# Optimization experiments

Hardware: AMD Instinct MI355X
Metric: run time of the kernel (lower is better)

The kernel has to match this reference:

```python
import jax, jax.numpy as jnp
import numpy as np

B, N, D_IN, D_MEM, LAYERS = 8, 2048, 128, 128, 3


def setup_inputs() -> dict:
    key = jax.random.key(0)
    k1, k2, k3, k4 = jax.random.split(key, 4)
    inputs = jax.random.normal(k1, (B, N, D_IN), dtype=jnp.float32)
    # attention-derived adjacency: nonnegative weights
    out_adj = jax.random.uniform(k2, (B, N, N), dtype=jnp.float32)
    # per-layer Linear weights (all layers 128->128 here, stacked) with
    # torch nn.Linear-style init scale 1/sqrt(fan_in)
    scale = 1.0 / np.sqrt(D_IN)
    W = jax.random.uniform(k3, (LAYERS, D_IN, D_MEM), minval=-scale, maxval=scale, dtype=jnp.float32)
    b = jax.random.uniform(k4, (LAYERS, D_MEM), minval=-scale, maxval=scale, dtype=jnp.float32)
    return {"inputs": inputs, "out_adj": out_adj, "W": W, "b": b}


def reference(inputs, out_adj, W, b):
    # GCN.forward (eval mode; dropout = identity)
    adj = out_adj  # [B, N, N]
    denom = jnp.sum(adj, axis=2, keepdims=True) + 1.0  # [B, N, 1]
    outputs = inputs  # [B, N, D]
    for l in range(W.shape[0]):
        Ax = jnp.einsum('bij,bjd->bid', adj, outputs)      # aggregate
        AxW = Ax @ W[l] + b[l]                             # per-layer linear
        outputs = jax.nn.relu(AxW / denom)                 # normalize + activate
    return outputs
```

## Files before the change

kernel.cpp:

```cpp
#include <hip/hip_runtime.h>

#define NN 2048
#define DD 128
#define BK 128
#define NT (NN / BK)

typedef _Float16 f16x8 __attribute__((ext_vector_type(8)));
typedef float f32x4 __attribute__((ext_vector_type(4)));

__global__ __launch_bounds__(256) void prep_kernel(
    const float* __restrict__ W, _Float16* __restrict__ Wt) {
  int idx = blockIdx.x * 256 + threadIdx.x;
  int l = idx >> 14, r = idx & 16383, d = r >> 7, k = r & 127;
  Wt[idx] = (_Float16)W[l * 16384 + k * 128 + d];
}

__global__ __launch_bounds__(256) void gemmY_kernel(
    const float* __restrict__ X, const _Float16* __restrict__ Wt,
    _Float16* __restrict__ Yt) {
  const int bx = blockIdx.x;
  const int batch = bx & 7, n0 = (bx >> 3) * 32;
  const int tid = threadIdx.x, lane = tid & 63, wave = tid >> 6;
  const int quad = lane >> 4, l15 = lane & 15, d0 = wave * 32;
  f32x4 acc[2][2] = {};
#pragma unroll
  for (int kk = 0; kk < 128; kk += 32) {
    f16x8 a0 = *(const f16x8*)(Wt + (d0 + l15) * DD + kk + quad * 8);
    f16x8 a1 = *(const f16x8*)(Wt + (d0 + 16 + l15) * DD + kk + quad * 8);
#pragma unroll
    for (int fi = 0; fi < 2; ++fi) {
      const float* xp = X + (size_t)(batch * NN + n0 + fi * 16 + l15) * DD + kk + quad * 8;
      float4 x0 = *(const float4*)xp;
      float4 x1 = *(const float4*)(xp + 4);
      f16x8 b = {(_Float16)x0.x, (_Float16)x0.y, (_Float16)x0.z, (_Float16)x0.w,
                 (_Float16)x1.x, (_Float16)x1.y, (_Float16)x1.z, (_Float16)x1.w};
      acc[0][fi] = __builtin_amdgcn_mfma_f32_16x16x32_f16(a0, b, acc[0][fi], 0, 0, 0);
      acc[1][fi] = __builtin_amdgcn_mfma_f32_16x16x32_f16(a1, b, acc[1][fi], 0, 0, 0);
    }
  }
  _Float16* YtB = Yt + (size_t)batch * DD * NN;
#pragma unroll
  for (int df = 0; df < 2; ++df)
#pragma unroll
    for (int fi = 0; fi < 2; ++fi)
#pragma unroll
      for (int r = 0; r < 4; ++r)
        YtB[(size_t)(d0 + df * 16 + quad * 4 + r) * NN + n0 + fi * 16 + l15] =
            (_Float16)acc[df][fi][r];
}

template<bool LAST>
__global__ __launch_bounds__(256, 2) void agg_kernel(
    const float* __restrict__ adj, const _Float16* __restrict__ Yt,
    const float* __restrict__ bias, const _Float16* __restrict__ Wn,
    _Float16* __restrict__ Ytn, float* __restrict__ out) {
  __shared__ __align__(16) float Bsm[2][32 * BK];
  float* acts = &Bsm[0][0];
  __shared__ float bsh[128];

  const int tid = threadIdx.x, bx = blockIdx.x;
  const int batch = bx & 7, i0 = (bx >> 3) * 32;
  const int wave = tid >> 6, lane = tid & 63;
  const int quad = lane >> 4, l15 = lane & 15;
  const int d0 = wave * 32;
  const int l31 = lane & 31, lh = lane >> 5;

  const float* adjB = adj + (size_t)(batch * NN + i0) * NN;
  const _Float16* YA0 = Yt + (size_t)batch * DD * NN + (size_t)(d0 + l15) * NN + quad * 8;
  const _Float16* YA1 = YA0 + (size_t)16 * NN;

  if (tid < 128) bsh[tid] = bias[tid];

  f32x4 acc[2][2] = {};
  float rs0 = 0.f, rs1 = 0.f;

  auto STAGE = [&](int ko, int buf) {
#pragma unroll
    for (int u = 0; u < 4; ++u) {
      const int rt = wave * 8 + u * 2 + lh;
      const float* g = adjB + (size_t)rt * NN + ko * BK + ((l31 ^ (rt & 7)) << 2);
      __builtin_amdgcn_global_load_lds(
          (const __attribute__((address_space(1))) unsigned int*)g,
          (__attribute__((address_space(3))) unsigned int*)
              &Bsm[buf][(wave * 8 + u * 2) * BK],
          16, 0, 0);
    }
  };

  STAGE(0, 0);
  __syncthreads();

  for (int ko = 0; ko < NT; ++ko) {
    const int buf = ko & 1;
    if (ko + 1 < NT) STAGE(ko + 1, buf ^ 1);
    f16x8 a[4][2];
#pragma unroll
    for (int kk = 0; kk < 4; ++kk) {
      a[kk][0] = *(const f16x8*)(YA0 + ko * BK + kk * 32);
      a[kk][1] = *(const f16x8*)(YA1 + ko * BK + kk * 32);
    }
    const float* Bt = Bsm[buf];
#pragma unroll
    for (int kk = 0; kk < 4; ++kk) {
#pragma unroll
      for (int fi = 0; fi < 2; ++fi) {
        const int row = fi * 16 + l15;
        const int c0 = kk * 8 + quad * 2;
        const float* rp = Bt + row * BK;
        float4 w0 = *(const float4*)(rp + ((c0 ^ (row & 7)) << 2));
        float4 w1 = *(const float4*)(rp + (((c0 + 1) ^ (row & 7)) << 2));
        float s = ((w0.x + w0.y) + (w0.z + w0.w)) + ((w1.x + w1.y) + (w1.z + w1.w));
        if (fi == 0) rs0 += s; else rs1 += s;
        f16x8 b = {(_Float16)w0.x, (_Float16)w0.y, (_Float16)w0.z, (_Float16)w0.w,
                   (_Float16)w1.x, (_Float16)w1.y, (_Float16)w1.z, (_Float16)w1.w};
        acc[0][fi] = __builtin_amdgcn_mfma_f32_16x16x32_f16(a[kk][0], b, acc[0][fi], 0, 0, 0);
        acc[1][fi] = __builtin_amdgcn_mfma_f32_16x16x32_f16(a[kk][1], b, acc[1][fi], 0, 0, 0);
      }
    }
    __syncthreads();
  }

  rs0 += __shfl_xor(rs0, 16); rs0 += __shfl_xor(rs0, 32);
  rs1 += __shfl_xor(rs1, 16); rs1 += __shfl_xor(rs1, 32);
  const float rdv0 = 1.0f / (rs0 + 1.0f);
  const float rdv1 = 1.0f / (rs1 + 1.0f);

#pragma unroll
  for (int af = 0; af < 2; ++af)
#pragma unroll
    for (int r = 0; r < 4; ++r) {
      const int d = d0 + af * 16 + quad * 4 + r;
      const float bv = bsh[d];
      acts[l15 * 132 + d]        = fmaxf((acc[af][0][r] + bv) * rdv0, 0.f);
      acts[(16 + l15) * 132 + d] = fmaxf((acc[af][1][r] + bv) * rdv1, 0.f);
    }
  __syncthreads();

  if (LAST) {
    float* ob = out + (size_t)(batch * NN + i0) * DD;
#pragma unroll
    for (int u = 0; u < 4; ++u) {
      int c = tid + 256 * u;
      int i = c >> 5, f4 = (c & 31) * 4;
      *(float4*)(ob + (size_t)i * DD + f4) = *(const float4*)&acts[i * 132 + f4];
    }
  } else {
    f32x4 acc2[2][2] = {};
#pragma unroll
    for (int kk = 0; kk < 128; kk += 32) {
      f16x8 a0 = *(const f16x8*)(Wn + (d0 + l15) * DD + kk + quad * 8);
      f16x8 a1 = *(const f16x8*)(Wn + (d0 + 16 + l15) * DD + kk + quad * 8);
#pragma unroll
      for (int fi = 0; fi < 2; ++fi) {
        const float* xp = &acts[(fi * 16 + l15) * 132 + kk + quad * 8];
        float4 x0 = *(const float4*)xp;
        float4 x1 = *(const float4*)(xp + 4);
        f16x8 b = {(_Float16)x0.x, (_Float16)x0.y, (_Float16)x0.z, (_Float16)x0.w,
                   (_Float16)x1.x, (_Float16)x1.y, (_Float16)x1.z, (_Float16)x1.w};
        acc2[0][fi] = __builtin_amdgcn_mfma_f32_16x16x32_f16(a0, b, acc2[0][fi], 0, 0, 0);
        acc2[1][fi] = __builtin_amdgcn_mfma_f32_16x16x32_f16(a1, b, acc2[1][fi], 0, 0, 0);
      }
    }
    _Float16* YnB = Ytn + (size_t)batch * DD * NN;
#pragma unroll
    for (int af = 0; af < 2; ++af)
#pragma unroll
      for (int fi = 0; fi < 2; ++fi)
#pragma unroll
        for (int r = 0; r < 4; ++r)
          YnB[(size_t)(d0 + af * 16 + quad * 4 + r) * NN + i0 + fi * 16 + l15] =
              (_Float16)acc2[af][fi][r];
  }
}

extern "C" void kernel_launch(void* const* d_in, const int* in_sizes, int n_in,
                              void* d_out, int out_size, void* d_ws, size_t ws_size,
                              hipStream_t stream) {
  const float* x0   = (const float*)d_in[0];
  const float* adj  = (const float*)d_in[1];
  const float* W    = (const float*)d_in[2];
  const float* bias = (const float*)d_in[3];
  float* out = (float*)d_out;

  char* ws = (char*)d_ws;
  _Float16* Wt  = (_Float16*)ws;
  _Float16* Yt0 = (_Float16*)(ws + (1u << 20));
  _Float16* Yt1 = (_Float16*)(ws + 6u * (1u << 20));

  prep_kernel <<<192, 256, 0, stream>>>(W, Wt);
  gemmY_kernel<<<512, 256, 0, stream>>>(x0, Wt, Yt0);
  agg_kernel<false><<<512, 256, 0, stream>>>(adj, Yt0, bias,       Wt + 16384, Yt1, nullptr);
  agg_kernel<false><<<512, 256, 0, stream>>>(adj, Yt1, bias + 128, Wt + 32768, Yt0, nullptr);
  agg_kernel<true ><<<512, 256, 0, stream>>>(adj, Yt0, bias + 256, nullptr,    nullptr, out);
}
```

Before: 303.4 us.

## Use single-wave agg blocks with register-prefetched global loads instead of LDS staging

```diff
diff --git a/kernel.cpp b/kernel.cpp
--- a/kernel.cpp
+++ b/kernel.cpp
@@ -2,8 +2,6 @@
 
 #define NN 2048
 #define DD 128
-#define BK 128
-#define NT (NN / BK)
 
 typedef _Float16 f16x8 __attribute__((ext_vector_type(8)));
 typedef float f32x4 __attribute__((ext_vector_type(4)));
@@ -50,126 +48,139 @@
 }
 
 template<bool LAST>
-__global__ __launch_bounds__(256, 2) void agg_kernel(
+__global__ __launch_bounds__(64, 1) void agg_kernel(
     const float* __restrict__ adj, const _Float16* __restrict__ Yt,
     const float* __restrict__ bias, const _Float16* __restrict__ Wn,
     _Float16* __restrict__ Ytn, float* __restrict__ out) {
-  __shared__ __align__(16) float Bsm[2][32 * BK];
-  float* acts = &Bsm[0][0];
-  __shared__ float bsh[128];
-
-  const int tid = threadIdx.x, bx = blockIdx.x;
+  __shared__ _Float16 acts[32][136];
+  __shared__ float rd[32];
+
+  const int bx = blockIdx.x;
   const int batch = bx & 7, i0 = (bx >> 3) * 32;
-  const int wave = tid >> 6, lane = tid & 63;
+  const int lane = threadIdx.x & 63;
   const int quad = lane >> 4, l15 = lane & 15;
-  const int d0 = wave * 32;
-  const int l31 = lane & 31, lh = lane >> 5;
-
-  const float* adjB = adj + (size_t)(batch * NN + i0) * NN;
-  const _Float16* YA0 = Yt + (size_t)batch * DD * NN + (size_t)(d0 + l15) * NN + quad * 8;
-  const _Float16* YA1 = YA0 + (size_t)16 * NN;
-
-  if (tid < 128) bsh[tid] = bias[tid];
-
-  f32x4 acc[2][2] = {};
+
+  const float* A0p = adj + (size_t)(batch * NN + i0 + l15) * NN + quad * 8;
+  const float* A1p = A0p + (size_t)16 * NN;
+  const _Float16* Yb = Yt + (size_t)batch * DD * NN + (size_t)l15 * NN + quad * 8;
+
+  f32x4 acc[2][8] = {};
   float rs0 = 0.f, rs1 = 0.f;
 
-  auto STAGE = [&](int ko, int buf) {
+  float4 pa[4][4];
+  f16x8 py[4][8];
+
+#define LOADS(jj, st)                                                   \
+  do {                                                                  \
+    pa[st][0] = *(const float4*)(A0p + (jj));                           \
+    pa[st][1] = *(const float4*)(A0p + (jj) + 4);                       \
+    pa[st][2] = *(const float4*)(A1p + (jj));                           \
+    pa[st][3] = *(const float4*)(A1p + (jj) + 4);                       \
+    _Pragma("unroll")                                                   \
+    for (int f = 0; f < 8; ++f)                                         \
+      py[st][f] = *(const f16x8*)(Yb + (size_t)(f * 16) * NN + (jj));   \
+  } while (0)
+
+#define COMPUTE(st)                                                     \
+  do {                                                                  \
+    float4 a00 = pa[st][0], a01 = pa[st][1];                            \
+    float4 a10 = pa[st][2], a11 = pa[st][3];                            \
+    f16x8 y[8];                                                         \
+    _Pragma("unroll")                                                   \
+    for (int f = 0; f < 8; ++f) y[f] = py[st][f];                       \
+    rs0 += ((a00.x + a00.y) + (a00.z + a00.w)) +                        \
+           ((a01.x + a01.y) + (a01.z + a01.w));                         \
+    rs1 += ((a10.x + a10.y) + (a10.z + a10.w)) +                        \
+           ((a11.x + a11.y) + (a11.z + a11.w));                         \
+    f16x8 af0 = {(_Float16)a00.x, (_Float16)a00.y, (_Float16)a00.z,     \
+                 (_Float16)a00.w, (_Float16)a01.x, (_Float16)a01.y,     \
+                 (_Float16)a01.z, (_Float16)a01.w};                     \
+    f16x8 af1 = {(_Float16)a10.x, (_Float16)a10.y, (_Float16)a10.z,     \
+                 (_Float16)a10.w, (_Float16)a11.x, (_Float16)a11.y,     \
+                 (_Float16)a11.z, (_Float16)a11.w};                     \
+    _Pragma("unroll")                                                   \
+    for (int f = 0; f < 8; ++f) {                                       \
+      acc[0][f] = __builtin_amdgcn_mfma_f32_16x16x32_f16(af0, y[f], acc[0][f], 0, 0, 0); \
+      acc[1][f] = __builtin_amdgcn_mfma_f32_16x16x32_f16(af1, y[f], acc[1][f], 0, 0, 0); \
+    }                                                                   \
+  } while (0)
+
+  LOADS(0, 0); LOADS(32, 1); LOADS(64, 2); LOADS(96, 3);
+
+  for (int j = 0; j < NN - 128; j += 128) {
 #pragma unroll
     for (int u = 0; u < 4; ++u) {
-      const int rt = wave * 8 + u * 2 + lh;
-      const float* g = adjB + (size_t)rt * NN + ko * BK + ((l31 ^ (rt & 7)) << 2);
-      __builtin_amdgcn_global_load_lds(
-          (const __attribute__((address_space(1))) unsigned int*)g,
-          (__attribute__((address_space(3))) unsigned int*)
-              &Bsm[buf][(wave * 8 + u * 2) * BK],
-          16, 0, 0);
+      COMPUTE(u);
+      LOADS(j + u * 32 + 128, u);
     }
-  };
-
-  STAGE(0, 0);
+  }
+#pragma unroll
+  for (int u = 0; u < 4; ++u) COMPUTE(u);
+#undef LOADS
+#undef COMPUTE
+
+  rs0 += __shfl_xor(rs0, 16); rs0 += __shfl_xor(rs0, 32);
+  rs1 += __shfl_xor(rs1, 16); rs1 += __shfl_xor(rs1, 32);
+  if (lane < 16) {
+    rd[l15] = 1.0f / (rs0 + 1.0f);
+    rd[16 + l15] = 1.0f / (rs1 + 1.0f);
+  }
   __syncthreads();
 
-  for (int ko = 0; ko < NT; ++ko) {
-    const int buf = ko & 1;
-    if (ko + 1 < NT) STAGE(ko + 1, buf ^ 1);
-    f16x8 a[4][2];
-#pragma unroll
-    for (int kk = 0; kk < 4; ++kk) {
-      a[kk][0] = *(const f16x8*)(YA0 + ko * BK + kk * 32);
-      a[kk][1] = *(const f16x8*)(YA1 + ko * BK + kk * 32);
-    }
-    const float* Bt = Bsm[buf];
-#pragma unroll
-    for (int kk = 0; kk < 4; ++kk) {
-#pragma unroll
-      for (int fi = 0; fi < 2; ++fi) {
-        const int row = fi * 16 + l15;
-        const int c0 = kk * 8 + quad * 2;
-        const float* rp = Bt + row * BK;
-        float4 w0 = *(const float4*)(rp + ((c0 ^ (row & 7)) << 2));
-        float4 w1 = *(const float4*)(rp + (((c0 + 1) ^ (row & 7)) << 2));
-        float s = ((w0.x + w0.y) + (w0.z + w0.w)) + ((w1.x + w1.y) + (w1.z + w1.w));
-        if (fi == 0) rs0 += s; else rs1 += s;
-        f16x8 b = {(_Float16)w0.x, (_Float16)w0.y, (_Float16)w0.z, (_Float16)w0.w,
-                   (_Float16)w1.x, (_Float16)w1.y, (_Float16)w1.z, (_Float16)w1.w};
-        acc[0][fi] = __builtin_amdgcn_mfma_f32_16x16x32_f16(a[kk][0], b, acc[0][fi], 0, 0, 0);
-        acc[1][fi] = __builtin_amdgcn_mfma_f32_16x16x32_f16(a[kk][1], b, acc[1][fi], 0, 0, 0);
+  float bv[8];
+#pragma unroll
+  for (int f = 0; f < 8; ++f) bv[f] = bias[f * 16 + l15];
+  float rdv[2][4];
+#pragma unroll
+  for (int fi = 0; fi < 2; ++fi)
+#pragma unroll
+    for (int r = 0; r < 4; ++r) rdv[fi][r] = rd[fi * 16 + quad * 4 + r];
+
+  if (LAST) {
+    float* ob = out + (size_t)(batch * NN + i0) * DD;
+#pragma unroll
+    for (int fi = 0; fi < 2; ++fi)
+#pragma unroll
+      for (int f = 0; f < 8; ++f)
+#pragma unroll
+        for (int r = 0; r < 4; ++r) {
+          int i = fi * 16 + quad * 4 + r;
+          ob[(size_t)i * DD + f * 16 + l15] =
+              fmaxf((acc[fi][f][r] + bv[f]) * rdv[fi][r], 0.f);
+        }
+  } else {
+#pragma unroll
+    for (int fi = 0; fi < 2; ++fi)
+#pragma unroll
+      for (int f = 0; f < 8; ++f)
+#pragma unroll
+        for (int r = 0; r < 4; ++r) {
+          int i = fi * 16 + quad * 4 + r;
+          acts[i][f * 16 + l15] =
+              (_Float16)fmaxf((acc[fi][f][r] + bv[f]) * rdv[fi][r], 0.f);
+        }
+    __syncthreads();
+    f32x4 acc2[8][2] = {};
+#pragma unroll
+    for (int kk = 0; kk < 128; kk += 32) {
+      f16x8 b0 = *(const f16x8*)&acts[l15][kk + quad * 8];
+      f16x8 b1 = *(const f16x8*)&acts[16 + l15][kk + quad * 8];
+#pragma unroll
+      for (int m = 0; m < 8; ++m) {
+        f16x8 aw = *(const f16x8*)(Wn + (m * 16 + l15) * DD + kk + quad * 8);
+        acc2[m][0] = __builtin_amdgcn_mfma_f32_16x16x32_f16(aw, b0, acc2[m][0], 0, 0, 0);
+        acc2[m][1] = __builtin_amdgcn_mfma_f32_16x16x32_f16(aw, b1, acc2[m][1], 0, 0, 0);
       }
     }
-    __syncthreads();
-  }
-
-  rs0 += __shfl_xor(rs0, 16); rs0 += __shfl_xor(rs0, 32);
-  rs1 += __shfl_xor(rs1, 16); rs1 += __shfl_xor(rs1, 32);
-  const float rdv0 = 1.0f / (rs0 + 1.0f);
-  const float rdv1 = 1.0f / (rs1 + 1.0f);
-
-#pragma unroll
-  for (int af = 0; af < 2; ++af)
-#pragma unroll
-    for (int r = 0; r < 4; ++r) {
-      const int d = d0 + af * 16 + quad * 4 + r;
-      const float bv = bsh[d];
-      acts[l15 * 132 + d]        = fmaxf((acc[af][0][r] + bv) * rdv0, 0.f);
-      acts[(16 + l15) * 132 + d] = fmaxf((acc[af][1][r] + bv) * rdv1, 0.f);
-    }
-  __syncthreads();
-
-  if (LAST) {
-    float* ob = out + (size_t)(batch * NN + i0) * DD;
-#pragma unroll
-    for (int u = 0; u < 4; ++u) {
-      int c = tid + 256 * u;
-      int i = c >> 5, f4 = (c & 31) * 4;
-      *(float4*)(ob + (size_t)i * DD + f4) = *(const float4*)&acts[i * 132 + f4];
-    }
-  } else {
-    f32x4 acc2[2][2] = {};
-#pragma unroll
-    for (int kk = 0; kk < 128; kk += 32) {
-      f16x8 a0 = *(const f16x8*)(Wn + (d0 + l15) * DD + kk + quad * 8);
-      f16x8 a1 = *(const f16x8*)(Wn + (d0 + 16 + l15) * DD + kk + quad * 8);
-#pragma unroll
-      for (int fi = 0; fi < 2; ++fi) {
-        const float* xp = &acts[(fi * 16 + l15) * 132 + kk + quad * 8];
-        float4 x0 = *(const float4*)xp;
-        float4 x1 = *(const float4*)(xp + 4);
-        f16x8 b = {(_Float16)x0.x, (_Float16)x0.y, (_Float16)x0.z, (_Float16)x0.w,
-                   (_Float16)x1.x, (_Float16)x1.y, (_Float16)x1.z, (_Float16)x1.w};
-        acc2[0][fi] = __builtin_amdgcn_mfma_f32_16x16x32_f16(a0, b, acc2[0][fi], 0, 0, 0);
-        acc2[1][fi] = __builtin_amdgcn_mfma_f32_16x16x32_f16(a1, b, acc2[1][fi], 0, 0, 0);
-      }
-    }
-    _Float16* YnB = Ytn + (size_t)batch * DD * NN;
-#pragma unroll
-    for (int af = 0; af < 2; ++af)
-#pragma unroll
-      for (int fi = 0; fi < 2; ++fi)
+    _Float16* Yn = Ytn + (size_t)batch * DD * NN;
+#pragma unroll
+    for (int m = 0; m < 8; ++m)
+#pragma unroll
+      for (int nf = 0; nf < 2; ++nf)
 #pragma unroll
         for (int r = 0; r < 4; ++r)
-          YnB[(size_t)(d0 + af * 16 + quad * 4 + r) * NN + i0 + fi * 16 + l15] =
-              (_Float16)acc2[af][fi][r];
+          Yn[(size_t)(m * 16 + quad * 4 + r) * NN + i0 + nf * 16 + l15] =
+              (_Float16)acc2[m][nf][r];
   }
 }
 
@@ -189,7 +200,7 @@
 
   prep_kernel <<<192, 256, 0, stream>>>(W, Wt);
   gemmY_kernel<<<512, 256, 0, stream>>>(x0, Wt, Yt0);
-  agg_kernel<false><<<512, 256, 0, stream>>>(adj, Yt0, bias,       Wt + 16384, Yt1, nullptr);
-  agg_kernel<false><<<512, 256, 0, stream>>>(adj, Yt1, bias + 128, Wt + 32768, Yt0, nullptr);
-  agg_kernel<true ><<<512, 256, 0, stream>>>(adj, Yt0, bias + 256, nullptr,    nullptr, out);
-}
+  agg_kernel<false><<<512, 64, 0, stream>>>(adj, Yt0, bias,       Wt + 16384, Yt1, nullptr);
+  agg_kernel<false><<<512, 64, 0, stream>>>(adj, Yt1, bias + 128, Wt + 32768, Yt0, nullptr);
+  agg_kernel<true ><<<512, 64, 0, stream>>>(adj, Yt0, bias + 256, nullptr,    nullptr, out);
+}
```

Result: slower. 348.9 us (+15.0%).
